# Performance work log

Measured on AMD Instinct MI355X. Metric: run time of the kernel, lower is better.

## Reference

```python
import jax, jax.numpy as jnp
import numpy as np

EPS = 1e-6


def box2corners(box):
    # box (N,5): x, y, w, h, alpha -> corners (N,4,2), CCW starting at (+w/2,+h/2)
    x, y, w, h, a = (box[:, i] for i in range(5))
    dx = jnp.array([0.5, -0.5, -0.5, 0.5], dtype=box.dtype)
    dy = jnp.array([0.5, 0.5, -0.5, -0.5], dtype=box.dtype)
    cx = dx[None, :] * w[:, None]
    cy = dy[None, :] * h[:, None]
    cos, sin = jnp.cos(a)[:, None], jnp.sin(a)[:, None]
    rx = cx * cos - cy * sin + x[:, None]
    ry = cx * sin + cy * cos + y[:, None]
    return jnp.stack([rx, ry], axis=-1)


def box_intersections(c1, c2):
    # Pairwise intersections of the 4 edges of box1 with the 4 edges of box2.
    # c1, c2: (N,4,2) -> points (N,16,2), valid mask (N,16)
    l1 = jnp.concatenate([c1, jnp.roll(c1, -1, axis=1)], axis=-1)[:, :, None, :]  # (N,4,1,4)
    l2 = jnp.concatenate([c2, jnp.roll(c2, -1, axis=1)], axis=-1)[:, None, :, :]  # (N,1,4,4)
    x1, y1, x2, y2 = (l1[..., i] for i in range(4))
    x3, y3, x4, y4 = (l2[..., i] for i in range(4))
    den = (x2 - x1) * (y4 - y3) - (y2 - y1) * (x4 - x3)
    den_safe = jnp.where(den == 0, 1.0, den)
    t = ((x3 - x1) * (y4 - y3) - (y3 - y1) * (x4 - x3)) / den_safe
    u = ((x3 - x1) * (y2 - y1) - (y3 - y1) * (x2 - x1)) / den_safe
    mask = (den != 0) & (t > 0.0) & (t < 1.0) & (u > 0.0) & (u < 1.0)
    px = x1 + t * (x2 - x1)
    py = y1 + t * (y2 - y1)
    pts = jnp.stack([px, py], axis=-1) * mask[..., None]
    N = c1.shape[0]
    return pts.reshape(N, 16, 2), mask.reshape(N, 16)


def corners_in_box(c1, c2):
    # Which corners of box1 lie inside box2, via projection onto box2 edges. (N,4) bool
    a = c2[:, 0:1]
    ab = c2[:, 1:2] - a
    ad = c2[:, 3:4] - a
    am = c1 - a  # (N,4,2)
    p_ab = (am * ab).sum(-1) / (ab * ab).sum(-1)
    p_ad = (am * ad).sum(-1) / (ad * ad).sum(-1)
    tol = 1e-6
    return (p_ab > -tol) & (p_ab < 1 + tol) & (p_ad > -tol) & (p_ad < 1 + tol)


def sorted_poly_area(pts, mask):
    # Sort valid vertices CCW around the valid-vertex mean, pad invalid slots with the
    # first sorted vertex (degenerate edges contribute 0), then shoelace area.
    # pts (N,M,2), mask (N,M) bool -> area (N,)
    maskf = mask.astype(pts.dtype)
    num = jnp.maximum(maskf.sum(-1, keepdims=True), 1.0)  # avoid /0 for empty polygons
    mean = (pts * maskf[..., None]).sum(1, keepdims=True) / num[..., None]
    centered = pts - mean
    ang = jnp.arctan2(centered[..., 1], centered[..., 0])
    ang = jnp.where(mask, ang, 1e9)  # invalid vertices sort last
    order = jnp.argsort(ang, axis=-1)
    sp = jnp.take_along_axis(pts, order[..., None], axis=1)
    sm = jnp.take_along_axis(mask, order, axis=1)
    sp = jnp.where(sm[..., None], sp, sp[:, 0:1])  # pad with first (valid) vertex
    nxt = jnp.roll(sp, -1, axis=1)
    cross = sp[..., 0] * nxt[..., 1] - sp[..., 1] * nxt[..., 0]
    return jnp.abs(cross.sum(-1)) * 0.5


def intersection_area(c1, c2):
    # Differentiable convex-polygon intersection area (Rotated_IoU style):
    # candidate vertices = corners of each box inside the other + edge intersections.
    ipts, imask = box_intersections(c1, c2)
    m1 = corners_in_box(c1, c2)
    m2 = corners_in_box(c2, c1)
    pts = jnp.concatenate([c1, c2, ipts], axis=1)    # (N,24,2)
    mask = jnp.concatenate([m1, m2, imask], axis=1)  # (N,24)
    return sorted_poly_area(pts, mask)


def poly_giou_loss(pred, target, weight):
    areas1 = pred[:, 2] * pred[:, 3]
    areas2 = target[:, 2] * target[:, 3]
    c1 = box2corners(pred)
    c2 = box2corners(target)
    overlap = intersection_area(c1, c2)
    union = areas1 + areas2 - overlap + EPS
    ious = jnp.maximum(overlap / union, EPS)
    # poly_enclose: all 8 corners, all valid
    all_pts = jnp.concatenate([c1, c2], axis=1)  # (N,8,2)
    enclose = sorted_poly_area(all_pts, jnp.ones(all_pts.shape[:2], bool))
    gious = ious - (enclose - union) / enclose
    loss = 1.0 - gious
    # weighted_loss with reduction='mean', avg_factor=None, loss_weight=1.0
    return (loss * weight).mean()


def setup_inputs() -> dict:
    key = jax.random.key(0)
    k1, k2, k3, k4, k5 = jax.random.split(key, 5)
    N = 500000
    xy = jax.random.uniform(k1, (N, 2), dtype=jnp.float32) * 100.0
    wh = jax.random.uniform(k2, (N, 2), dtype=jnp.float32) * 10.0 + 1.0
    ang = (jax.random.uniform(k3, (N, 1), dtype=jnp.float32) - 0.5) * np.float32(np.pi)
    pred = jnp.concatenate([xy, wh, ang], axis=-1)
    noise = jax.random.normal(k4, (N, 5), dtype=jnp.float32) * jnp.array(
        [1.0, 1.0, 0.5, 0.5, 0.1], dtype=jnp.float32)
    target = pred + noise
    target = target.at[:, 2:4].set(jnp.maximum(target[:, 2:4], 0.5))
    weight = jax.random.uniform(k5, (N,), dtype=jnp.float32)
    return {"pred": pred, "target": target, "weight": weight}


def reference(pred, target, weight):
    return poly_giou_loss(pred, target, weight)
```

## Files before the change

### kernel.cpp

```cpp
#include <hip/hip_runtime.h>
#include <math.h>

#define BLOCK 256

__device__ __forceinline__ float fast_rcp(float x) {
    return __builtin_amdgcn_rcpf(x);
}
__device__ __forceinline__ float fsin(float x) {
    return __builtin_amdgcn_sinf(x * 0.15915494309189535f);
}
__device__ __forceinline__ float fcos(float x) {
    return __builtin_amdgcn_cosf(x * 0.15915494309189535f);
}

__device__ __forceinline__ float pseudo_angle(float x, float y) {
    float d = fabsf(x) + fabsf(y);
    float p = (d == 0.f) ? 1.f : x * fast_rcp(d);
    return (y < 0.f) ? (p - 1.f) : (1.f - p);
}

struct Shoe {
    float sfx, sfy, spx, spy, acc;
    bool have;
};

__device__ __forceinline__ void emit(Shoe& s, bool c, float X, float Y) {
    float cr = s.spx * Y - s.spy * X;
    s.acc += (c && s.have) ? cr : 0.f;
    s.sfx = (c && !s.have) ? X : s.sfx;
    s.sfy = (c && !s.have) ? Y : s.sfy;
    s.spx = c ? X : s.spx;
    s.spy = c ? Y : s.spy;
    s.have = s.have || c;
}

__device__ __forceinline__ void edge_clip_y(Shoe& s, bool en, float ax, float ay,
                                            float bx, float by, float hh) {
    bool inA = en && (ay <= hh) && (ay >= -hh);
    bool cA = en && ((ay > hh) != (by > hh));
    bool cB = en && ((ay < -hh) != (by < -hh));
    float dxe = bx - ax, dye = by - ay;
    float rd = fast_rcp(dye);
    float tA = (hh - ay) * rd;
    float tB = (-hh - ay) * rd;
    float xA = fmaf(tA, dxe, ax);
    float xB = fmaf(tB, dxe, ax);
    bool fA = cA && (!cB || (tA <= tB));
    float e1x = fA ? xA : xB, e1y = fA ? hh : -hh;
    float e2x = fA ? xB : xA, e2y = fA ? -hh : hh;
    emit(s, inA, ax, ay);
    emit(s, cA || cB, e1x, e1y);
    emit(s, cA && cB, e2x, e2y);
}

__device__ __forceinline__ float box_loss(const float* __restrict__ pred,
                                          const float* __restrict__ target,
                                          const float* __restrict__ weight, int i) {
    float p[5], q[5];
#pragma unroll
    for (int j = 0; j < 5; ++j) p[j] = pred[i * 5 + j];
#pragma unroll
    for (int j = 0; j < 5; ++j) q[j] = target[i * 5 + j];
    float wgt = weight[i];

    float cq = fcos(q[4]), sq = fsin(q[4]);
    float dang = p[4] - q[4];
    float cd = fcos(dang), sd = fsin(dang);
    float hw = 0.5f * q[2], hh = 0.5f * q[3];
    float dxc = p[0] - q[0], dyc = p[1] - q[1];
    float tx = dxc * cq + dyc * sq;
    float ty = -dxc * sq + dyc * cq;
    float ax_ = 0.5f * p[2] * cd, ay_ = 0.5f * p[2] * sd;
    float bx_ = -0.5f * p[3] * sd, by_ = 0.5f * p[3] * cd;

    float qx[4], qy[4];
    qx[0] = tx + ax_ + bx_; qy[0] = ty + ay_ + by_;
    qx[1] = tx - ax_ + bx_; qy[1] = ty - ay_ + by_;
    qx[2] = tx - ax_ - bx_; qy[2] = ty - ay_ - by_;
    qx[3] = tx + ax_ - bx_; qy[3] = ty + ay_ - by_;

    float sxk[8], syk[8];
    bool sv[8];
#pragma unroll
    for (int e = 0; e < 4; ++e) {
        int en = (e + 1) & 3;
        float xc = qx[e], yc = qy[e], xn = qx[en], yn = qy[en];
        float dxe = xn - xc, dye = yn - yc;
        bool inC = (xc <= hw) && (xc >= -hw);
        bool cA = (xc > hw) != (xn > hw);
        bool cB = (xc < -hw) != (xn < -hw);
        float rd = fast_rcp(dxe);
        float tA = (hw - xc) * rd;
        float tB = (-hw - xc) * rd;
        float yA = fmaf(tA, dye, yc);
        float yB = fmaf(tB, dye, yc);
        bool fA = cA && (!cB || (tA <= tB));
        float X1x = fA ? hw : -hw, X1y = fA ? yA : yB;
        float X2x = fA ? -hw : hw, X2y = fA ? yB : yA;
        sxk[2 * e]     = inC ? xc : X1x;
        syk[2 * e]     = inC ? yc : X1y;
        sv[2 * e]      = inC || cA || cB;
        sxk[2 * e + 1] = inC ? X1x : X2x;
        syk[2 * e + 1] = inC ? X1y : X2y;
        sv[2 * e + 1]  = inC ? (cA || cB) : (cA && cB);
    }

    Shoe sh; sh.sfx = sh.sfy = sh.spx = sh.spy = sh.acc = 0.f; sh.have = false;
    bool have_p = false;
    float pfx = 0.f, pfy = 0.f, pvx = 0.f, pvy = 0.f;
#pragma unroll
    for (int k = 0; k < 8; ++k) {
        bool val = sv[k];
        float cx_ = sxk[k], cy_ = syk[k];
        edge_clip_y(sh, have_p && val, pvx, pvy, cx_, cy_, hh);
        pfx = (val && !have_p) ? cx_ : pfx;
        pfy = (val && !have_p) ? cy_ : pfy;
        pvx = val ? cx_ : pvx;
        pvy = val ? cy_ : pvy;
        have_p = have_p || val;
    }
    edge_clip_y(sh, have_p, pvx, pvy, pfx, pfy, hh);
    float wrap = sh.spx * sh.sfy - sh.spy * sh.sfx;
    float accs = sh.acc + (sh.have ? wrap : 0.f);
    float overlap = 0.5f * fabsf(accs);

    float enc;
    {
        float px8[8], py8[8];
#pragma unroll
        for (int j = 0; j < 4; ++j) { px8[j] = qx[j]; py8[j] = qy[j]; }
        px8[4] = hw;  py8[4] = hh;
        px8[5] = -hw; py8[5] = hh;
        px8[6] = -hw; py8[6] = -hh;
        px8[7] = hw;  py8[7] = -hh;
        float ex = 0.f, ey = 0.f;
#pragma unroll
        for (int j = 0; j < 8; ++j) { ex += px8[j]; ey += py8[j]; }
        float mx = ex * 0.125f, my = ey * 0.125f;
        float ang[8];
#pragma unroll
        for (int j = 0; j < 8; ++j) ang[j] = pseudo_angle(px8[j] - mx, py8[j] - my);

#define CE(I, J)                                                   \
        {                                                          \
            bool sw = ang[I] > ang[J];                             \
            float ta = sw ? ang[J] : ang[I];                       \
            float tb = sw ? ang[I] : ang[J];                       \
            ang[I] = ta; ang[J] = tb;                              \
            float txp = sw ? px8[J] : px8[I];                      \
            float typ = sw ? py8[J] : py8[I];                      \
            px8[J] = sw ? px8[I] : px8[J];                         \
            py8[J] = sw ? py8[I] : py8[J];                         \
            px8[I] = txp; py8[I] = typ;                            \
        }
        CE(0,1) CE(2,3) CE(4,5) CE(6,7)
        CE(0,2) CE(1,3) CE(4,6) CE(5,7)
        CE(1,2) CE(5,6)
        CE(0,4) CE(1,5) CE(2,6) CE(3,7)
        CE(2,4) CE(3,5)
        CE(1,2) CE(3,4) CE(5,6)
#undef CE

        float acc2 = 0.f;
#pragma unroll
        for (int k = 0; k < 8; ++k) {
            int kn = (k + 1) & 7;
            acc2 += px8[k] * py8[kn] - py8[k] * px8[kn];
        }
        enc = 0.5f * fabsf(acc2);
    }

    float area1 = p[2] * p[3];
    float area2 = q[2] * q[3];
    float uni = area1 + area2 - overlap + 1e-6f;
    float iou = fmaxf(overlap / uni, 1e-6f);
    float giou = iou - (enc - uni) / enc;
    return (1.f - giou) * wgt;
}

__launch_bounds__(BLOCK)
__global__ void giou_kernel(const float* __restrict__ pred,
                            const float* __restrict__ target,
                            const float* __restrict__ weight,
                            float* __restrict__ partials, int N, int half) {
    int tid = threadIdx.x;
    int gi = blockIdx.x * BLOCK + tid;
    int i1 = (gi < half) ? gi : (half - 1);
    int i2 = i1 + half;
    bool v1 = (gi < half);
    bool v2 = v1 && (i2 < N);
    i2 = v2 ? i2 : i1;

    float l1 = box_loss(pred, target, weight, i1);
    float l2 = box_loss(pred, target, weight, i2);
    float loss = (v1 ? l1 : 0.f) + (v2 ? l2 : 0.f);

#pragma unroll
    for (int off = 32; off > 0; off >>= 1)
        loss += __shfl_down(loss, off, 64);
    if ((tid & 63) == 0)
        partials[blockIdx.x * (BLOCK / 64) + (tid >> 6)] = loss;
}

__launch_bounds__(1024)
__global__ void reduce_kernel(const float* __restrict__ partials,
                              float* __restrict__ out, int nparts, float scale) {
    __shared__ float acc[16];
    int tid = threadIdx.x;
    float s = 0.f;
    for (int j = tid; j < nparts; j += 1024) s += partials[j];
#pragma unroll
    for (int off = 32; off > 0; off >>= 1)
        s += __shfl_down(s, off, 64);
    if ((tid & 63) == 0) acc[tid >> 6] = s;
    __syncthreads();
    if (tid == 0) {
        float t = 0.f;
#pragma unroll
        for (int k = 0; k < 16; ++k) t += acc[k];
        out[0] = t * scale;
    }
}

extern "C" void kernel_launch(void* const* d_in, const int* in_sizes, int n_in,
                              void* d_out, int out_size, void* d_ws, size_t ws_size,
                              hipStream_t stream) {
    const float* pred   = (const float*)d_in[0];
    const float* target = (const float*)d_in[1];
    const float* weight = (const float*)d_in[2];
    float* out = (float*)d_out;
    float* ws  = (float*)d_ws;
    int N = in_sizes[0] / 5;
    int half = (N + 1) / 2;

    int nblocks = (half + BLOCK - 1) / BLOCK;
    int nparts = nblocks * (BLOCK / 64);
    giou_kernel<<<nblocks, BLOCK, 0, stream>>>(pred, target, weight, ws, N, half);
    reduce_kernel<<<1, 1024, 0, stream>>>(ws, out, nparts, 1.0f / (float)N);
}
```

Measured before the change: 82.55 us.

## Compute overlap area via Green's theorem on clipped edges instead of polygon clipping

Replaces the sequential Sutherland-Hodgman clip-and-shoelace of the intersection polygon with an edge-wise sum. Each box edge is clipped to the other box (Liang-Barsky against the axis-aligned box, Cyrus-Beck against the rotated quad) and its cross-product contribution is added. This removes the serial vertex-chaining state and its dependency chain. It also drops the two-boxes-per-thread scheme for one box per thread, which changes ILP and launch size, and degenerate or tangent cases may be handled slightly differently.

```diff
diff --git a/kernel.cpp b/kernel.cpp
--- a/kernel.cpp
+++ b/kernel.cpp
@@ -19,43 +19,71 @@
     return (y < 0.f) ? (p - 1.f) : (1.f - p);
 }
 
-struct Shoe {
-    float sfx, sfy, spx, spy, acc;
-    bool have;
-};
-
-__device__ __forceinline__ void emit(Shoe& s, bool c, float X, float Y) {
-    float cr = s.spx * Y - s.spy * X;
-    s.acc += (c && s.have) ? cr : 0.f;
-    s.sfx = (c && !s.have) ? X : s.sfx;
-    s.sfy = (c && !s.have) ? Y : s.sfy;
-    s.spx = c ? X : s.spx;
-    s.spy = c ? Y : s.spy;
-    s.have = s.have || c;
-}
-
-__device__ __forceinline__ void edge_clip_y(Shoe& s, bool en, float ax, float ay,
-                                            float bx, float by, float hh) {
-    bool inA = en && (ay <= hh) && (ay >= -hh);
-    bool cA = en && ((ay > hh) != (by > hh));
-    bool cB = en && ((ay < -hh) != (by < -hh));
-    float dxe = bx - ax, dye = by - ay;
-    float rd = fast_rcp(dye);
-    float tA = (hh - ay) * rd;
-    float tB = (-hh - ay) * rd;
-    float xA = fmaf(tA, dxe, ax);
-    float xB = fmaf(tB, dxe, ax);
-    bool fA = cA && (!cB || (tA <= tB));
-    float e1x = fA ? xA : xB, e1y = fA ? hh : -hh;
-    float e2x = fA ? xB : xA, e2y = fA ? -hh : hh;
-    emit(s, inA, ax, ay);
-    emit(s, cA || cB, e1x, e1y);
-    emit(s, cA && cB, e2x, e2y);
-}
-
-__device__ __forceinline__ float box_loss(const float* __restrict__ pred,
-                                          const float* __restrict__ target,
-                                          const float* __restrict__ weight, int i) {
+__device__ __forceinline__ float seg_in_aabb_cross(float ax, float ay,
+                                                   float bx, float by,
+                                                   float hw, float hh) {
+    float ex = bx - ax, ey = by - ay;
+    float t0 = 0.f, t1 = 1.f;
+    bool feas = true;
+    {
+        bool par = (ex == 0.f);
+        float r = fast_rcp(ex);
+        float ta = (hw - ax) * r, tb = (-hw - ax) * r;
+        float tlo = fminf(ta, tb), thi = fmaxf(ta, tb);
+        t0 = par ? t0 : fmaxf(t0, tlo);
+        t1 = par ? t1 : fminf(t1, thi);
+        feas = feas && (!par || (fabsf(ax) <= hw));
+    }
+    {
+        bool par = (ey == 0.f);
+        float r = fast_rcp(ey);
+        float ta = (hh - ay) * r, tb = (-hh - ay) * r;
+        float tlo = fminf(ta, tb), thi = fmaxf(ta, tb);
+        t0 = par ? t0 : fmaxf(t0, tlo);
+        t1 = par ? t1 : fminf(t1, thi);
+        feas = feas && (!par || (fabsf(ay) <= hh));
+    }
+    bool valid = feas && (t1 > t0);
+    float pax = fmaf(t0, ex, ax), pay = fmaf(t0, ey, ay);
+    float pbx = fmaf(t1, ex, ax), pby = fmaf(t1, ey, ay);
+    float cr = pax * pby - pay * pbx;
+    return valid ? cr : 0.f;
+}
+
+__device__ __forceinline__ float seg_in_quad_cross(float ax, float ay,
+                                                   float ex, float ey,
+                                                   const float* qx,
+                                                   const float* qy) {
+    float t0 = 0.f, t1 = 1.f;
+    bool feas = true;
+#pragma unroll
+    for (int i = 0; i < 4; ++i) {
+        int in_ = (i + 1) & 3;
+        float dix = qx[in_] - qx[i], diy = qy[in_] - qy[i];
+        float ga = dix * (ay - qy[i]) - diy * (ax - qx[i]);
+        float gd = dix * ey - diy * ex;
+        bool par = (gd == 0.f);
+        float tk = -ga * fast_rcp(gd);
+        t0 = (!par && gd > 0.f) ? fmaxf(t0, tk) : t0;
+        t1 = (!par && gd < 0.f) ? fminf(t1, tk) : t1;
+        feas = feas && (!par || (ga >= 0.f));
+    }
+    bool valid = feas && (t1 > t0);
+    float pax = fmaf(t0, ex, ax), pay = fmaf(t0, ey, ay);
+    float pbx = fmaf(t1, ex, ax), pby = fmaf(t1, ey, ay);
+    float cr = pax * pby - pay * pbx;
+    return valid ? cr : 0.f;
+}
+
+__launch_bounds__(BLOCK)
+__global__ void giou_kernel(const float* __restrict__ pred,
+                            const float* __restrict__ target,
+                            const float* __restrict__ weight,
+                            float* __restrict__ partials, int N) {
+    int tid = threadIdx.x;
+    long gi = (long)blockIdx.x * BLOCK + tid;
+    int i = (gi < (long)N) ? (int)gi : (N - 1);
+
     float p[5], q[5];
 #pragma unroll
     for (int j = 0; j < 5; ++j) p[j] = pred[i * 5 + j];
@@ -79,50 +107,17 @@
     qx[2] = tx - ax_ - bx_; qy[2] = ty - ay_ - by_;
     qx[3] = tx + ax_ - bx_; qy[3] = ty + ay_ - by_;
 
-    float sxk[8], syk[8];
-    bool sv[8];
-#pragma unroll
-    for (int e = 0; e < 4; ++e) {
-        int en = (e + 1) & 3;
-        float xc = qx[e], yc = qy[e], xn = qx[en], yn = qy[en];
-        float dxe = xn - xc, dye = yn - yc;
-        bool inC = (xc <= hw) && (xc >= -hw);
-        bool cA = (xc > hw) != (xn > hw);
-        bool cB = (xc < -hw) != (xn < -hw);
-        float rd = fast_rcp(dxe);
-        float tA = (hw - xc) * rd;
-        float tB = (-hw - xc) * rd;
-        float yA = fmaf(tA, dye, yc);
-        float yB = fmaf(tB, dye, yc);
-        bool fA = cA && (!cB || (tA <= tB));
-        float X1x = fA ? hw : -hw, X1y = fA ? yA : yB;
-        float X2x = fA ? -hw : hw, X2y = fA ? yB : yA;
-        sxk[2 * e]     = inC ? xc : X1x;
-        syk[2 * e]     = inC ? yc : X1y;
-        sv[2 * e]      = inC || cA || cB;
-        sxk[2 * e + 1] = inC ? X1x : X2x;
-        syk[2 * e + 1] = inC ? X1y : X2y;
-        sv[2 * e + 1]  = inC ? (cA || cB) : (cA && cB);
-    }
-
-    Shoe sh; sh.sfx = sh.sfy = sh.spx = sh.spy = sh.acc = 0.f; sh.have = false;
-    bool have_p = false;
-    float pfx = 0.f, pfy = 0.f, pvx = 0.f, pvy = 0.f;
-#pragma unroll
-    for (int k = 0; k < 8; ++k) {
-        bool val = sv[k];
-        float cx_ = sxk[k], cy_ = syk[k];
-        edge_clip_y(sh, have_p && val, pvx, pvy, cx_, cy_, hh);
-        pfx = (val && !have_p) ? cx_ : pfx;
-        pfy = (val && !have_p) ? cy_ : pfy;
-        pvx = val ? cx_ : pvx;
-        pvy = val ? cy_ : pvy;
-        have_p = have_p || val;
-    }
-    edge_clip_y(sh, have_p, pvx, pvy, pfx, pfy, hh);
-    float wrap = sh.spx * sh.sfy - sh.spy * sh.sfx;
-    float accs = sh.acc + (sh.have ? wrap : 0.f);
-    float overlap = 0.5f * fabsf(accs);
+    float s = 0.f;
+    s += seg_in_aabb_cross(qx[0], qy[0], qx[1], qy[1], hw, hh);
+    s += seg_in_aabb_cross(qx[1], qy[1], qx[2], qy[2], hw, hh);
+    s += seg_in_aabb_cross(qx[2], qy[2], qx[3], qy[3], hw, hh);
+    s += seg_in_aabb_cross(qx[3], qy[3], qx[0], qy[0], hw, hh);
+    float w2 = hw + hw, h2 = hh + hh;
+    s += seg_in_quad_cross(hw, -hh, 0.f, h2, qx, qy);
+    s += seg_in_quad_cross(hw, hh, -w2, 0.f, qx, qy);
+    s += seg_in_quad_cross(-hw, hh, 0.f, -h2, qx, qy);
+    s += seg_in_quad_cross(-hw, -hh, w2, 0.f, qx, qy);
+    float overlap = 0.5f * fabsf(s);
 
     float enc;
     {
@@ -175,25 +170,8 @@
     float uni = area1 + area2 - overlap + 1e-6f;
     float iou = fmaxf(overlap / uni, 1e-6f);
     float giou = iou - (enc - uni) / enc;
-    return (1.f - giou) * wgt;
-}
-
-__launch_bounds__(BLOCK)
-__global__ void giou_kernel(const float* __restrict__ pred,
-                            const float* __restrict__ target,
-                            const float* __restrict__ weight,
-                            float* __restrict__ partials, int N, int half) {
-    int tid = threadIdx.x;
-    int gi = blockIdx.x * BLOCK + tid;
-    int i1 = (gi < half) ? gi : (half - 1);
-    int i2 = i1 + half;
-    bool v1 = (gi < half);
-    bool v2 = v1 && (i2 < N);
-    i2 = v2 ? i2 : i1;
-
-    float l1 = box_loss(pred, target, weight, i1);
-    float l2 = box_loss(pred, target, weight, i2);
-    float loss = (v1 ? l1 : 0.f) + (v2 ? l2 : 0.f);
+    float loss = (1.f - giou) * wgt;
+    if (gi >= (long)N) loss = 0.f;
 
 #pragma unroll
     for (int off = 32; off > 0; off >>= 1)
@@ -231,10 +209,9 @@
     float* out = (float*)d_out;
     float* ws  = (float*)d_ws;
     int N = in_sizes[0] / 5;
-    int half = (N + 1) / 2;
-
-    int nblocks = (half + BLOCK - 1) / BLOCK;
+
+    int nblocks = (N + BLOCK - 1) / BLOCK;
     int nparts = nblocks * (BLOCK / 64);
-    giou_kernel<<<nblocks, BLOCK, 0, stream>>>(pred, target, weight, ws, N, half);
+    giou_kernel<<<nblocks, BLOCK, 0, stream>>>(pred, target, weight, ws, N);
     reduce_kernel<<<1, 1024, 0, stream>>>(ws, out, nparts, 1.0f / (float)N);
 }
```

After: 82.31 us. About the same (-0.3%).
